# Optimization experiments

Hardware: AMD Instinct MI355X
Metric: run time of the kernel (lower is better)

Reference implementation:

```python
import jax, jax.numpy as jnp
import numpy as np


def setup_inputs() -> dict:
    key = jax.random.key(0)
    B, H, S, D = 4, 16, 2048, 128  # batch, kv heads, seq_len, head_dim
    kv_cache = jax.random.normal(key, (B, H, S, D), dtype=jnp.float32)
    return {"kv_cache": kv_cache, "rank": 64}


def reference(kv_cache, rank):
    # compress(): batched reduced SVD, truncate to `rank` components.
    orig_shape = kv_cache.shape
    S_len, D = orig_shape[-2], orig_shape[-1]
    x = kv_cache.reshape(-1, S_len, D)                 # [N, S, D]
    U, s, Vh = jnp.linalg.svd(x, full_matrices=False)  # U:[N,S,D], s:[N,D], Vh:[N,D,D]
    U_t = U[:, :, :rank]                               # [N, S, r]
    s_t = s[:, :rank]                                  # [N, r]
    Vh_t = Vh[:, :rank, :]                             # [N, r, D]
    left = U_t * s_t[:, None, :]                       # [N, S, r]  (= U * diag(s))
    # decompress(): left @ right^T, right = V[:, :, :rank] so right^T = Vh_t
    reconstructed = jnp.matmul(left, Vh_t)             # [N, S, D]
    return reconstructed.reshape(orig_shape)
```

## Files before the change

kernel.cpp:

```cpp
#include <hip/hip_runtime.h>


#define NM 64
#define SEQ 2048
#define DD 128
#define RR 64
#define NSWEEP 7
#define NROUND (NSWEEP * 64)

#define OFF_VFULL (4194304ULL)
#define OFF_NORM  (8388608ULL)
#define OFF_VT    (33554432ULL)

__device__ __forceinline__ float dot4(float4 a, float4 b) {
  return a.x * b.x + a.y * b.y + a.z * b.z + a.w * b.w;
}

template <int CTRL>
__device__ __forceinline__ float dpp_add(float x) {
  int y = __builtin_amdgcn_update_dpp(0, __float_as_int(x), CTRL, 0xf, 0xf, true);
  return x + __int_as_float(y);
}
__device__ __forceinline__ float red8(float x) {
  x = dpp_add<0xB1>(x);
  x = dpp_add<0x4E>(x);
  x = dpp_add<0x141>(x);
  return x;
}

__device__ __forceinline__ void jrot(float app, float apq, float aqq,
                                     float& c, float& s) {
  c = 1.f;
  s = 0.f;
  if (apq * apq > 1e-9f * app * aqq) {
    float tau = (aqq - app) / (2.f * apq);
    float tv = 1.f / (fabsf(tau) + sqrtf(1.f + tau * tau));
    tv = tau < 0.f ? -tv : tv;
    c = 1.f / sqrtf(1.f + tv * tv);
    s = tv * c;
  }
}

__device__ __forceinline__ void rot4(float c, float s, float4 p, float4 q,
                                     float4& np, float4& nq) {
  np.x = c * p.x - s * q.x;  nq.x = s * p.x + c * q.x;
  np.y = c * p.y - s * q.y;  nq.y = s * p.y + c * q.y;
  np.z = c * p.z - s * q.z;  nq.z = s * p.z + c * q.z;
  np.w = c * p.w - s * q.w;  nq.w = s * p.w + c * q.w;
}

__global__ __launch_bounds__(256) void gram_k(const float* __restrict__ X,
                                              float* __restrict__ G) {
  const int m = blockIdx.y;
  const int r0 = blockIdx.x * 32;
  const int tid = threadIdx.x;
  __shared__ __align__(16) float Xs[64][128];
  const float* Xm = X + (size_t)m * SEQ * DD;
  const int ti = tid >> 5;
  const int tj = tid & 31;
  float acc[4][4];
#pragma unroll
  for (int a = 0; a < 4; ++a)
#pragma unroll
    for (int b = 0; b < 4; ++b) acc[a][b] = 0.f;

  for (int s0 = 0; s0 < SEQ; s0 += 64) {
    __syncthreads();
    for (int t = tid; t < 2048; t += 256) {
      int s = t >> 5, c4 = t & 31;
      *(float4*)&Xs[s][c4 * 4] =
          *(const float4*)&Xm[(size_t)(s0 + s) * DD + c4 * 4];
    }
    __syncthreads();
#pragma unroll 4
    for (int s = 0; s < 64; ++s) {
      float4 av = *(const float4*)&Xs[s][r0 + 4 * ti];
      float4 bv = *(const float4*)&Xs[s][4 * tj];
      acc[0][0] += av.x * bv.x; acc[0][1] += av.x * bv.y;
      acc[0][2] += av.x * bv.z; acc[0][3] += av.x * bv.w;
      acc[1][0] += av.y * bv.x; acc[1][1] += av.y * bv.y;
      acc[1][2] += av.y * bv.z; acc[1][3] += av.y * bv.w;
      acc[2][0] += av.z * bv.x; acc[2][1] += av.z * bv.y;
      acc[2][2] += av.z * bv.z; acc[2][3] += av.z * bv.w;
      acc[3][0] += av.w * bv.x; acc[3][1] += av.w * bv.y;
      acc[3][2] += av.w * bv.z; acc[3][3] += av.w * bv.w;
    }
  }
  float* Gm = G + (size_t)m * DD * DD;
#pragma unroll
  for (int a = 0; a < 4; ++a) {
    float4 v = make_float4(acc[a][0], acc[a][1], acc[a][2], acc[a][3]);
    *(float4*)&Gm[(size_t)(r0 + 4 * ti + a) * DD + 4 * tj] = v;
  }
}

__global__ __launch_bounds__(512) void jacobi_oe_k(const float* __restrict__ G,
                                                   float* __restrict__ Vfull,
                                                   float* __restrict__ normg) {
  const int m = blockIdx.x;
  const int tid = threadIdx.x;
  const int g = tid >> 3;
  const int l = tid & 7;
  __shared__ float4 xch[DD * 32];

  const float4* Gm4 = (const float4*)(G + (size_t)m * DD * DD);
  float4 ce[4], co[4];
#pragma unroll
  for (int j = 0; j < 4; ++j) {
    ce[j] = Gm4[(size_t)(2 * g) * 32 + l + 8 * j];
    co[j] = Gm4[(size_t)(2 * g + 1) * 32 + l + 8 * j];
  }
  const bool hasR = (g < 63);
  const bool hasL = (g > 0);
  float4* homeE = &xch[(2 * g) * 32];
  float4* homeR = &xch[(2 * g + 2) * 32];

  for (int round = 0; round < NROUND; ++round) {
    {
      float app = 0.f, apq = 0.f, aqq = 0.f;
#pragma unroll
      for (int j = 0; j < 4; ++j) {
        app += dot4(ce[j], ce[j]);
        apq += dot4(ce[j], co[j]);
        aqq += dot4(co[j], co[j]);
      }
      app = red8(app); apq = red8(apq); aqq = red8(aqq);
      float c, s;
      jrot(app, apq, aqq, c, s);
#pragma unroll
      for (int j = 0; j < 4; ++j) {
        float4 np, nq;
        rot4(c, s, ce[j], co[j], np, nq);
        ce[j] = nq;
        co[j] = np;
      }
    }
    if (hasL) {
#pragma unroll
      for (int j = 0; j < 4; ++j) homeE[l + 8 * j] = ce[j];
    }
    __syncthreads();
    if (hasR) {
      float4 r[4];
#pragma unroll
      for (int j = 0; j < 4; ++j) r[j] = homeR[l + 8 * j];
      float app = 0.f, apq = 0.f, aqq = 0.f;
#pragma unroll
      for (int j = 0; j < 4; ++j) {
        app += dot4(co[j], co[j]);
        apq += dot4(co[j], r[j]);
        aqq += dot4(r[j], r[j]);
      }
      app = red8(app); apq = red8(apq); aqq = red8(aqq);
      float c, s;
      jrot(app, apq, aqq, c, s);
#pragma unroll
      for (int j = 0; j < 4; ++j) {
        float4 np, nq;
        rot4(c, s, co[j], r[j], np, nq);
        homeR[l + 8 * j] = np;
        co[j] = nq;
      }
    }
    __syncthreads();
    if (hasL) {
#pragma unroll
      for (int j = 0; j < 4; ++j) ce[j] = homeE[l + 8 * j];
    }
  }

  float ne = 0.f, no = 0.f;
#pragma unroll
  for (int j = 0; j < 4; ++j) {
    ne += dot4(ce[j], ce[j]);
    no += dot4(co[j], co[j]);
  }
  ne = red8(ne);
  no = red8(no);
  float4* Ve = (float4*)(Vfull + ((size_t)m * DD + 2 * g) * DD);
  float4* Vo = (float4*)(Vfull + ((size_t)m * DD + 2 * g + 1) * DD);
#pragma unroll
  for (int j = 0; j < 4; ++j) {
    Ve[l + 8 * j] = ce[j];
    Vo[l + 8 * j] = co[j];
  }
  if (l == 0) {
    normg[m * DD + 2 * g] = ne;
    normg[m * DD + 2 * g + 1] = no;
  }
}

__global__ __launch_bounds__(128) void select_k(const float* __restrict__ Vfull,
                                                const float* __restrict__ normg,
                                                float* __restrict__ Vt) {
  const int m = blockIdx.x;
  const int t = threadIdx.x;
  __shared__ float n[DD];
  __shared__ int inv[RR];
  __shared__ float scl[RR];
  n[t] = normg[m * DD + t];
  __syncthreads();
  float nt = n[t];
  int rk = 0;
  for (int k = 0; k < DD; ++k) {
    float nk = n[k];
    rk += ((nk > nt) || (nk == nt && k < t)) ? 1 : 0;
  }
  if (rk < RR) { inv[rk] = t; scl[rk] = 1.f / sqrtf(nt); }
  __syncthreads();
  for (int r = 0; r < RR; ++r) {
    Vt[((size_t)m * RR + r) * DD + t] =
        Vfull[((size_t)m * DD + inv[r]) * DD + t] * scl[r];
  }
}

__global__ __launch_bounds__(256) void gemm1_k(const float* __restrict__ X,
                                               const float* __restrict__ Vt,
                                               float* __restrict__ W) {
  const int m = blockIdx.y;
  const int s0 = blockIdx.x * 32;
  const int tid = threadIdx.x;
  __shared__ __align__(16) float VtT[128 * 68];
  __shared__ __align__(16) float Xs[32 * 132];
  const float* Vm = Vt + (size_t)m * RR * DD;
  for (int t = tid; t < RR * DD; t += 256) {
    int r = t >> 7, c = t & 127;
    VtT[c * 68 + r] = Vm[t];
  }
  const float* Xm = X + ((size_t)m * SEQ + s0) * DD;
  for (int t = tid; t < 1024; t += 256) {
    int s = t >> 5, c4 = t & 31;
    *(float4*)&Xs[s * 132 + 4 * c4] = *(const float4*)&Xm[(size_t)s * DD + 4 * c4];
  }
  __syncthreads();
  const int ti = tid >> 4;
  const int tj = tid & 15;
  float acc[2][4] = {{0.f, 0.f, 0.f, 0.f}, {0.f, 0.f, 0.f, 0.f}};
#pragma unroll 4
  for (int k = 0; k < DD; ++k) {
    float a0 = Xs[(2 * ti) * 132 + k];
    float a1 = Xs[(2 * ti + 1) * 132 + k];
    float4 bv = *(float4*)&VtT[k * 68 + 4 * tj];
    acc[0][0] += a0 * bv.x; acc[0][1] += a0 * bv.y;
    acc[0][2] += a0 * bv.z; acc[0][3] += a0 * bv.w;
    acc[1][0] += a1 * bv.x; acc[1][1] += a1 * bv.y;
    acc[1][2] += a1 * bv.z; acc[1][3] += a1 * bv.w;
  }
  float* Wm = W + ((size_t)m * SEQ + s0) * RR;
#pragma unroll
  for (int d = 0; d < 2; ++d) {
    float4 v = make_float4(acc[d][0], acc[d][1], acc[d][2], acc[d][3]);
    *(float4*)&Wm[(size_t)(2 * ti + d) * RR + 4 * tj] = v;
  }
}

__global__ __launch_bounds__(256) void gemm2_k(const float* __restrict__ W,
                                               const float* __restrict__ Vt,
                                               float* __restrict__ out) {
  const int m = blockIdx.y;
  const int s0 = blockIdx.x * 32;
  const int tid = threadIdx.x;
  __shared__ __align__(16) float Vts[64 * 132];
  __shared__ __align__(16) float Ws[32 * 68];
  const float* Vm = Vt + (size_t)m * RR * DD;
  for (int t = tid; t < 2048; t += 256) {
    int r = t >> 5, c4 = t & 31;
    *(float4*)&Vts[r * 132 + 4 * c4] = *(const float4*)&Vm[(size_t)r * DD + 4 * c4];
  }
  const float* Wm = W + ((size_t)m * SEQ + s0) * RR;
  for (int t = tid; t < 512; t += 256) {
    int s = t >> 4, c4 = t & 15;
    *(float4*)&Ws[s * 68 + 4 * c4] = *(const float4*)&Wm[(size_t)s * RR + 4 * c4];
  }
  __syncthreads();
  const int ti = tid >> 5;
  const int tj = tid & 31;
  float acc[4][4] = {{0.f,0.f,0.f,0.f},{0.f,0.f,0.f,0.f},
                     {0.f,0.f,0.f,0.f},{0.f,0.f,0.f,0.f}};
#pragma unroll 4
  for (int k = 0; k < RR; ++k) {
    float4 bv = *(float4*)&Vts[k * 132 + 4 * tj];
    float a0 = Ws[(4 * ti + 0) * 68 + k];
    float a1 = Ws[(4 * ti + 1) * 68 + k];
    float a2 = Ws[(4 * ti + 2) * 68 + k];
    float a3 = Ws[(4 * ti + 3) * 68 + k];
    acc[0][0] += a0 * bv.x; acc[0][1] += a0 * bv.y;
    acc[0][2] += a0 * bv.z; acc[0][3] += a0 * bv.w;
    acc[1][0] += a1 * bv.x; acc[1][1] += a1 * bv.y;
    acc[1][2] += a1 * bv.z; acc[1][3] += a1 * bv.w;
    acc[2][0] += a2 * bv.x; acc[2][1] += a2 * bv.y;
    acc[2][2] += a2 * bv.z; acc[2][3] += a2 * bv.w;
    acc[3][0] += a3 * bv.x; acc[3][1] += a3 * bv.y;
    acc[3][2] += a3 * bv.z; acc[3][3] += a3 * bv.w;
  }
  float* Om = out + ((size_t)m * SEQ + s0) * DD;
#pragma unroll
  for (int d = 0; d < 4; ++d) {
    float4 v = make_float4(acc[d][0], acc[d][1], acc[d][2], acc[d][3]);
    *(float4*)&Om[(size_t)(4 * ti + d) * DD + 4 * tj] = v;
  }
}

extern "C" void kernel_launch(void* const* d_in, const int* in_sizes, int n_in,
                              void* d_out, int out_size, void* d_ws, size_t ws_size,
                              hipStream_t stream) {
  (void)in_sizes; (void)n_in; (void)out_size; (void)ws_size;
  const float* X = (const float*)d_in[0];
  float* out = (float*)d_out;
  char* ws = (char*)d_ws;
  float* G = (float*)ws;
  float* Vfull = (float*)(ws + OFF_VFULL);
  float* normg = (float*)(ws + OFF_NORM);
  float* Vt = (float*)(ws + OFF_VT);
  float* W = (float*)ws;

  gram_k<<<dim3(4, NM), 256, 0, stream>>>(X, G);
  jacobi_oe_k<<<NM, 512, 0, stream>>>(G, Vfull, normg);
  select_k<<<NM, 128, 0, stream>>>(Vfull, normg, Vt);
  gemm1_k<<<dim3(SEQ / 32, NM), 256, 0, stream>>>(X, Vt, W);
  gemm2_k<<<dim3(SEQ / 32, NM), 256, 0, stream>>>(W, Vt, out);
}
```

Baseline: 1.132 ms.

## Replace odd-even Jacobi with hierarchical block Jacobi using wave-local exchanges

Replaces the flat odd-even one-sided Jacobi (448 rounds, each with two block-wide barriers) with a hierarchical scheme. Each 64-thread wavefront runs intra-block odd-even and ring rotations among its 16 columns, synchronising through LDS with only an lgkmcnt wait and no block barrier. Block-wide __syncthreads is needed only when blocks are swapped between waves in a 16-block tournament. This cuts the barrier count sharply and skips rotation arithmetic when the off-diagonal term is negligible, at the cost of a different sweep ordering and possibly different convergence or accuracy with the same cycle count.

Result: slower. 1.212 ms (+7.1%).

```diff
diff --git a/kernel.cpp b/kernel.cpp
--- a/kernel.cpp
+++ b/kernel.cpp
@@ -5,8 +5,7 @@
 #define SEQ 2048
 #define DD 128
 #define RR 64
-#define NSWEEP 7
-#define NROUND (NSWEEP * 64)
+#define NCYC 7
 
 #define OFF_VFULL (4194304ULL)
 #define OFF_NORM  (8388608ULL)
@@ -28,17 +27,20 @@
   return x;
 }
 
-__device__ __forceinline__ void jrot(float app, float apq, float aqq,
+__device__ __forceinline__ void waitlds() {
+  asm volatile("s_waitcnt lgkmcnt(0)" ::: "memory");
+  __builtin_amdgcn_sched_barrier(0);
+}
+
+__device__ __forceinline__ bool jrot(float app, float apq, float aqq,
                                      float& c, float& s) {
-  c = 1.f;
-  s = 0.f;
-  if (apq * apq > 1e-9f * app * aqq) {
-    float tau = (aqq - app) / (2.f * apq);
-    float tv = 1.f / (fabsf(tau) + sqrtf(1.f + tau * tau));
-    tv = tau < 0.f ? -tv : tv;
-    c = 1.f / sqrtf(1.f + tv * tv);
-    s = tv * c;
-  }
+  if (apq * apq <= 1e-9f * app * aqq) return false;
+  float tau = (aqq - app) / (2.f * apq);
+  float tv = 1.f / (fabsf(tau) + sqrtf(1.f + tau * tau));
+  tv = tau < 0.f ? -tv : tv;
+  c = 1.f / sqrtf(1.f + tv * tv);
+  s = tv * c;
+  return true;
 }
 
 __device__ __forceinline__ void rot4(float c, float s, float4 p, float4 q,
@@ -94,99 +96,166 @@
   }
 }
 
-__global__ __launch_bounds__(512) void jacobi_oe_k(const float* __restrict__ G,
-                                                   float* __restrict__ Vfull,
-                                                   float* __restrict__ normg) {
+__global__ __launch_bounds__(512) void jacobi_hier_k(const float* __restrict__ G,
+                                                     float* __restrict__ Vfull,
+                                                     float* __restrict__ normg) {
   const int m = blockIdx.x;
   const int tid = threadIdx.x;
-  const int g = tid >> 3;
+  const int W = tid >> 6;
+  const int o = (tid >> 3) & 7;
   const int l = tid & 7;
-  __shared__ float4 xch[DD * 32];
+  __shared__ float4 buf[4096];
+  float4* M = &buf[W * 264];
 
   const float4* Gm4 = (const float4*)(G + (size_t)m * DD * DD);
   float4 ce[4], co[4];
 #pragma unroll
   for (int j = 0; j < 4; ++j) {
-    ce[j] = Gm4[(size_t)(2 * g) * 32 + l + 8 * j];
-    co[j] = Gm4[(size_t)(2 * g + 1) * 32 + l + 8 * j];
-  }
-  const bool hasR = (g < 63);
-  const bool hasL = (g > 0);
-  float4* homeE = &xch[(2 * g) * 32];
-  float4* homeR = &xch[(2 * g + 2) * 32];
-
-  for (int round = 0; round < NROUND; ++round) {
-    {
-      float app = 0.f, apq = 0.f, aqq = 0.f;
+    ce[j] = Gm4[(size_t)(8 * W + o) * 32 + l + 8 * j];
+    co[j] = Gm4[(size_t)(8 * (15 - W) + o) * 32 + l + 8 * j];
+  }
+  const int dst_ce = (W == 0) ? 0 : W + 1;
+  const int dst_co = (W == 0) ? 1 : 16 - W;
+
+#pragma unroll 1
+  for (int cyc = 0; cyc < NCYC; ++cyc) {
+#pragma unroll 1
+    for (int r = 0; r < 8; ++r) {
+      {
+        float app = 0.f, apq = 0.f, aqq = 0.f;
+#pragma unroll
+        for (int j = 0; j < 4; ++j) {
+          app += dot4(ce[j], ce[j]);
+          apq += dot4(ce[j], co[j]);
+          aqq += dot4(co[j], co[j]);
+        }
+        app = red8(app); apq = red8(apq); aqq = red8(aqq);
+        float c, s;
+        if (jrot(app, apq, aqq, c, s)) {
+#pragma unroll
+          for (int j = 0; j < 4; ++j) {
+            float4 np, nq;
+            rot4(c, s, ce[j], co[j], np, nq);
+            ce[j] = nq; co[j] = np;
+          }
+        } else {
+#pragma unroll
+          for (int j = 0; j < 4; ++j) { float4 t = ce[j]; ce[j] = co[j]; co[j] = t; }
+        }
+      }
+      if (o > 0) {
+#pragma unroll
+        for (int j = 0; j < 4; ++j) M[o * 33 + l + 8 * j] = ce[j];
+      }
+      waitlds();
+      if (o < 7) {
+        float4 r4[4];
+#pragma unroll
+        for (int j = 0; j < 4; ++j) r4[j] = M[(o + 1) * 33 + l + 8 * j];
+        float app = 0.f, apq = 0.f, aqq = 0.f;
+#pragma unroll
+        for (int j = 0; j < 4; ++j) {
+          app += dot4(co[j], co[j]);
+          apq += dot4(co[j], r4[j]);
+          aqq += dot4(r4[j], r4[j]);
+        }
+        app = red8(app); apq = red8(apq); aqq = red8(aqq);
+        float c, s;
+        if (jrot(app, apq, aqq, c, s)) {
+#pragma unroll
+          for (int j = 0; j < 4; ++j) {
+            float4 np, nq;
+            rot4(c, s, co[j], r4[j], np, nq);
+            M[(o + 1) * 33 + l + 8 * j] = np;
+            co[j] = nq;
+          }
+        } else {
+#pragma unroll
+          for (int j = 0; j < 4; ++j) {
+            M[(o + 1) * 33 + l + 8 * j] = co[j];
+            co[j] = r4[j];
+          }
+        }
+      }
+      waitlds();
+      if (o > 0) {
+#pragma unroll
+        for (int j = 0; j < 4; ++j) ce[j] = M[o * 33 + l + 8 * j];
+      }
+    }
+#pragma unroll
+    for (int j = 0; j < 4; ++j) { float4 t = ce[j]; ce[j] = co[j]; co[j] = t; }
+
+#pragma unroll 1
+    for (int st = 0; st < 15; ++st) {
+      float4 qv[4];
+#pragma unroll
+      for (int j = 0; j < 4; ++j) qv[j] = co[j];
+#pragma unroll 1
+      for (int k = 0; k < 8; ++k) {
+        float app = 0.f, apq = 0.f, aqq = 0.f;
+#pragma unroll
+        for (int j = 0; j < 4; ++j) {
+          app += dot4(ce[j], ce[j]);
+          apq += dot4(ce[j], qv[j]);
+          aqq += dot4(qv[j], qv[j]);
+        }
+        app = red8(app); apq = red8(apq); aqq = red8(aqq);
+        float c, s;
+        if (jrot(app, apq, aqq, c, s)) {
+#pragma unroll
+          for (int j = 0; j < 4; ++j) {
+            float4 np, nq;
+            rot4(c, s, ce[j], qv[j], np, nq);
+            ce[j] = np; qv[j] = nq;
+          }
+        }
+        if (k < 7) {
+#pragma unroll
+          for (int j = 0; j < 4; ++j) M[o * 33 + l + 8 * j] = qv[j];
+          waitlds();
+#pragma unroll
+          for (int j = 0; j < 4; ++j) qv[j] = M[((o + 1) & 7) * 33 + l + 8 * j];
+        }
+      }
+#pragma unroll
+      for (int j = 0; j < 4; ++j) co[j] = qv[j];
+
+      __syncthreads();
 #pragma unroll
       for (int j = 0; j < 4; ++j) {
-        app += dot4(ce[j], ce[j]);
-        apq += dot4(ce[j], co[j]);
-        aqq += dot4(co[j], co[j]);
-      }
-      app = red8(app); apq = red8(apq); aqq = red8(aqq);
-      float c, s;
-      jrot(app, apq, aqq, c, s);
+        buf[dst_ce * 256 + o * 32 + l + 8 * j] = ce[j];
+        buf[dst_co * 256 + o * 32 + l + 8 * j] = co[j];
+      }
+      __syncthreads();
 #pragma unroll
       for (int j = 0; j < 4; ++j) {
-        float4 np, nq;
-        rot4(c, s, ce[j], co[j], np, nq);
-        ce[j] = nq;
-        co[j] = np;
-      }
+        ce[j] = buf[W * 256 + o * 32 + l + 8 * j];
+        co[j] = buf[(15 - W) * 256 + o * 32 + l + 8 * j];
+      }
+      __syncthreads();
     }
-    if (hasL) {
-#pragma unroll
-      for (int j = 0; j < 4; ++j) homeE[l + 8 * j] = ce[j];
-    }
-    __syncthreads();
-    if (hasR) {
-      float4 r[4];
-#pragma unroll
-      for (int j = 0; j < 4; ++j) r[j] = homeR[l + 8 * j];
-      float app = 0.f, apq = 0.f, aqq = 0.f;
-#pragma unroll
-      for (int j = 0; j < 4; ++j) {
-        app += dot4(co[j], co[j]);
-        apq += dot4(co[j], r[j]);
-        aqq += dot4(r[j], r[j]);
-      }
-      app = red8(app); apq = red8(apq); aqq = red8(aqq);
-      float c, s;
-      jrot(app, apq, aqq, c, s);
-#pragma unroll
-      for (int j = 0; j < 4; ++j) {
-        float4 np, nq;
-        rot4(c, s, co[j], r[j], np, nq);
-        homeR[l + 8 * j] = np;
-        co[j] = nq;
-      }
-    }
-    __syncthreads();
-    if (hasL) {
-#pragma unroll
-      for (int j = 0; j < 4; ++j) ce[j] = homeE[l + 8 * j];
-    }
-  }
-
-  float ne = 0.f, no = 0.f;
+  }
+
+  float ne = 0.f, no_ = 0.f;
 #pragma unroll
   for (int j = 0; j < 4; ++j) {
     ne += dot4(ce[j], ce[j]);
-    no += dot4(co[j], co[j]);
+    no_ += dot4(co[j], co[j]);
   }
   ne = red8(ne);
-  no = red8(no);
-  float4* Ve = (float4*)(Vfull + ((size_t)m * DD + 2 * g) * DD);
-  float4* Vo = (float4*)(Vfull + ((size_t)m * DD + 2 * g + 1) * DD);
+  no_ = red8(no_);
+  const int ie = W * 16 + 2 * o;
+  float4* Ve = (float4*)(Vfull + ((size_t)m * DD + ie) * DD);
+  float4* Vo = (float4*)(Vfull + ((size_t)m * DD + ie + 1) * DD);
 #pragma unroll
   for (int j = 0; j < 4; ++j) {
     Ve[l + 8 * j] = ce[j];
     Vo[l + 8 * j] = co[j];
   }
   if (l == 0) {
-    normg[m * DD + 2 * g] = ne;
-    normg[m * DD + 2 * g + 1] = no;
+    normg[m * DD + ie] = ne;
+    normg[m * DD + ie + 1] = no_;
   }
 }
 
@@ -315,7 +384,7 @@
   float* W = (float*)ws;
 
   gram_k<<<dim3(4, NM), 256, 0, stream>>>(X, G);
-  jacobi_oe_k<<<NM, 512, 0, stream>>>(G, Vfull, normg);
+  jacobi_hier_k<<<NM, 512, 0, stream>>>(G, Vfull, normg);
   select_k<<<NM, 128, 0, stream>>>(Vfull, normg, Vt);
   gemm1_k<<<dim3(SEQ / 32, NM), 256, 0, stream>>>(X, Vt, W);
   gemm2_k<<<dim3(SEQ / 32, NM), 256, 0, stream>>>(W, Vt, out);
```

## Process two matrices per Jacobi block and make rotation computation branch-free

Applied to the files above, without the earlier changes.

The Jacobi eigen-solver kernel now handles two independent Gram matrices per 512-thread block, interleaving their dot products, reductions and rotations so each barrier and DPP-reduction latency is amortized over twice the independent work. The exchange buffer is also halved to hold only even columns per matrix. The rotation helper is rewritten with selects instead of a branch to avoid divergence. The cost is double register pressure per thread and only 32 blocks launched, which leaves many CUs idle on a 256-CU device.

After: 2.035 ms. +79.8%, slower.

```diff
diff --git a/kernel.cpp b/kernel.cpp
--- a/kernel.cpp
+++ b/kernel.cpp
@@ -30,15 +30,15 @@
 
 __device__ __forceinline__ void jrot(float app, float apq, float aqq,
                                      float& c, float& s) {
-  c = 1.f;
-  s = 0.f;
-  if (apq * apq > 1e-9f * app * aqq) {
-    float tau = (aqq - app) / (2.f * apq);
-    float tv = 1.f / (fabsf(tau) + sqrtf(1.f + tau * tau));
-    tv = tau < 0.f ? -tv : tv;
-    c = 1.f / sqrtf(1.f + tv * tv);
-    s = tv * c;
-  }
+  bool ok = apq * apq > 1e-9f * app * aqq;
+  float ap = ok ? apq : 1.f;
+  float tau = (aqq - app) / (2.f * ap);
+  float tv = 1.f / (fabsf(tau) + sqrtf(1.f + tau * tau));
+  tv = tau < 0.f ? -tv : tv;
+  float cc = 1.f / sqrtf(1.f + tv * tv);
+  float ss = tv * cc;
+  c = ok ? cc : 1.f;
+  s = ok ? ss : 0.f;
 }
 
 __device__ __forceinline__ void rot4(float c, float s, float4 p, float4 q,
@@ -94,99 +94,133 @@
   }
 }
 
-__global__ __launch_bounds__(512) void jacobi_oe_k(const float* __restrict__ G,
-                                                   float* __restrict__ Vfull,
-                                                   float* __restrict__ normg) {
-  const int m = blockIdx.x;
+__global__ __launch_bounds__(512) void jacobi2_k(const float* __restrict__ G,
+                                                 float* __restrict__ Vfull,
+                                                 float* __restrict__ normg) {
+  const int m0 = 2 * blockIdx.x;
+  const int m1 = 2 * blockIdx.x + 1;
   const int tid = threadIdx.x;
   const int g = tid >> 3;
   const int l = tid & 7;
-  __shared__ float4 xch[DD * 32];
-
-  const float4* Gm4 = (const float4*)(G + (size_t)m * DD * DD);
-  float4 ce[4], co[4];
+  __shared__ __align__(16) float4 xA[RR * 32];
+  __shared__ __align__(16) float4 xB[RR * 32];
+
+  const float4* GA = (const float4*)(G + (size_t)m0 * DD * DD);
+  const float4* GB = (const float4*)(G + (size_t)m1 * DD * DD);
+  float4 ceA[4], coA[4], ceB[4], coB[4];
 #pragma unroll
   for (int j = 0; j < 4; ++j) {
-    ce[j] = Gm4[(size_t)(2 * g) * 32 + l + 8 * j];
-    co[j] = Gm4[(size_t)(2 * g + 1) * 32 + l + 8 * j];
+    ceA[j] = GA[(size_t)(2 * g) * 32 + l + 8 * j];
+    coA[j] = GA[(size_t)(2 * g + 1) * 32 + l + 8 * j];
+    ceB[j] = GB[(size_t)(2 * g) * 32 + l + 8 * j];
+    coB[j] = GB[(size_t)(2 * g + 1) * 32 + l + 8 * j];
   }
   const bool hasR = (g < 63);
   const bool hasL = (g > 0);
-  float4* homeE = &xch[(2 * g) * 32];
-  float4* homeR = &xch[(2 * g + 2) * 32];
+  float4* hEA = &xA[g * 32];
+  float4* hRA = &xA[(g + 1) * 32];
+  float4* hEB = &xB[g * 32];
+  float4* hRB = &xB[(g + 1) * 32];
 
   for (int round = 0; round < NROUND; ++round) {
     {
-      float app = 0.f, apq = 0.f, aqq = 0.f;
-#pragma unroll
-      for (int j = 0; j < 4; ++j) {
-        app += dot4(ce[j], ce[j]);
-        apq += dot4(ce[j], co[j]);
-        aqq += dot4(co[j], co[j]);
-      }
-      app = red8(app); apq = red8(apq); aqq = red8(aqq);
-      float c, s;
-      jrot(app, apq, aqq, c, s);
+      float apA = 0.f, aqA = 0.f, axA = 0.f;
+      float apB = 0.f, aqB = 0.f, axB = 0.f;
+#pragma unroll
+      for (int j = 0; j < 4; ++j) {
+        apA += dot4(ceA[j], ceA[j]); axA += dot4(ceA[j], coA[j]);
+        aqA += dot4(coA[j], coA[j]);
+        apB += dot4(ceB[j], ceB[j]); axB += dot4(ceB[j], coB[j]);
+        aqB += dot4(coB[j], coB[j]);
+      }
+      apA = red8(apA); axA = red8(axA); aqA = red8(aqA);
+      apB = red8(apB); axB = red8(axB); aqB = red8(aqB);
+      float cA, sA, cB, sB;
+      jrot(apA, axA, aqA, cA, sA);
+      jrot(apB, axB, aqB, cB, sB);
 #pragma unroll
       for (int j = 0; j < 4; ++j) {
         float4 np, nq;
-        rot4(c, s, ce[j], co[j], np, nq);
-        ce[j] = nq;
-        co[j] = np;
+        rot4(cA, sA, ceA[j], coA[j], np, nq);
+        ceA[j] = nq; coA[j] = np;
+        rot4(cB, sB, ceB[j], coB[j], np, nq);
+        ceB[j] = nq; coB[j] = np;
       }
     }
     if (hasL) {
 #pragma unroll
-      for (int j = 0; j < 4; ++j) homeE[l + 8 * j] = ce[j];
+      for (int j = 0; j < 4; ++j) {
+        hEA[l + 8 * j] = ceA[j];
+        hEB[l + 8 * j] = ceB[j];
+      }
     }
     __syncthreads();
     if (hasR) {
-      float4 r[4];
-#pragma unroll
-      for (int j = 0; j < 4; ++j) r[j] = homeR[l + 8 * j];
-      float app = 0.f, apq = 0.f, aqq = 0.f;
-#pragma unroll
-      for (int j = 0; j < 4; ++j) {
-        app += dot4(co[j], co[j]);
-        apq += dot4(co[j], r[j]);
-        aqq += dot4(r[j], r[j]);
-      }
-      app = red8(app); apq = red8(apq); aqq = red8(aqq);
-      float c, s;
-      jrot(app, apq, aqq, c, s);
+      float4 rA[4], rB[4];
+#pragma unroll
+      for (int j = 0; j < 4; ++j) {
+        rA[j] = hRA[l + 8 * j];
+        rB[j] = hRB[l + 8 * j];
+      }
+      float apA = 0.f, aqA = 0.f, axA = 0.f;
+      float apB = 0.f, aqB = 0.f, axB = 0.f;
+#pragma unroll
+      for (int j = 0; j < 4; ++j) {
+        apA += dot4(coA[j], coA[j]); axA += dot4(coA[j], rA[j]);
+        aqA += dot4(rA[j], rA[j]);
+        apB += dot4(coB[j], coB[j]); axB += dot4(coB[j], rB[j]);
+        aqB += dot4(rB[j], rB[j]);
+      }
+      apA = red8(apA); axA = red8(axA); aqA = red8(aqA);
+      apB = red8(apB); axB = red8(axB); aqB = red8(aqB);
+      float cA, sA, cB, sB;
+      jrot(apA, axA, aqA, cA, sA);
+      jrot(apB, axB, aqB, cB, sB);
 #pragma unroll
       for (int j = 0; j < 4; ++j) {
         float4 np, nq;
-        rot4(c, s, co[j], r[j], np, nq);
-        homeR[l + 8 * j] = np;
-        co[j] = nq;
+        rot4(cA, sA, coA[j], rA[j], np, nq);
+        hRA[l + 8 * j] = np;
+        coA[j] = nq;
+        rot4(cB, sB, coB[j], rB[j], np, nq);
+        hRB[l + 8 * j] = np;
+        coB[j] = nq;
       }
     }
     __syncthreads();
     if (hasL) {
 #pragma unroll
-      for (int j = 0; j < 4; ++j) ce[j] = homeE[l + 8 * j];
-    }
-  }
-
-  float ne = 0.f, no = 0.f;
+      for (int j = 0; j < 4; ++j) {
+        ceA[j] = hEA[l + 8 * j];
+        ceB[j] = hEB[l + 8 * j];
+      }
+    }
+  }
+
+  float nA0 = 0.f, nA1 = 0.f, nB0 = 0.f, nB1 = 0.f;
 #pragma unroll
   for (int j = 0; j < 4; ++j) {
-    ne += dot4(ce[j], ce[j]);
-    no += dot4(co[j], co[j]);
-  }
-  ne = red8(ne);
-  no = red8(no);
-  float4* Ve = (float4*)(Vfull + ((size_t)m * DD + 2 * g) * DD);
-  float4* Vo = (float4*)(Vfull + ((size_t)m * DD + 2 * g + 1) * DD);
+    nA0 += dot4(ceA[j], ceA[j]); nA1 += dot4(coA[j], coA[j]);
+    nB0 += dot4(ceB[j], ceB[j]); nB1 += dot4(coB[j], coB[j]);
+  }
+  nA0 = red8(nA0); nA1 = red8(nA1);
+  nB0 = red8(nB0); nB1 = red8(nB1);
+  float4* VeA = (float4*)(Vfull + ((size_t)m0 * DD + 2 * g) * DD);
+  float4* VoA = (float4*)(Vfull + ((size_t)m0 * DD + 2 * g + 1) * DD);
+  float4* VeB = (float4*)(Vfull + ((size_t)m1 * DD + 2 * g) * DD);
+  float4* VoB = (float4*)(Vfull + ((size_t)m1 * DD + 2 * g + 1) * DD);
 #pragma unroll
   for (int j = 0; j < 4; ++j) {
-    Ve[l + 8 * j] = ce[j];
-    Vo[l + 8 * j] = co[j];
+    VeA[l + 8 * j] = ceA[j];
+    VoA[l + 8 * j] = coA[j];
+    VeB[l + 8 * j] = ceB[j];
+    VoB[l + 8 * j] = coB[j];
   }
   if (l == 0) {
-    normg[m * DD + 2 * g] = ne;
-    normg[m * DD + 2 * g + 1] = no;
+    normg[m0 * DD + 2 * g] = nA0;
+    normg[m0 * DD + 2 * g + 1] = nA1;
+    normg[m1 * DD + 2 * g] = nB0;
+    normg[m1 * DD + 2 * g + 1] = nB1;
   }
 }
 
@@ -315,7 +349,7 @@
   float* W = (float*)ws;
 
   gram_k<<<dim3(4, NM), 256, 0, stream>>>(X, G);
-  jacobi_oe_k<<<NM, 512, 0, stream>>>(G, Vfull, normg);
+  jacobi2_k<<<NM / 2, 512, 0, stream>>>(G, Vfull, normg);
   select_k<<<NM, 128, 0, stream>>>(Vfull, normg, Vt);
   gemm1_k<<<dim3(SEQ / 32, NM), 256, 0, stream>>>(X, Vt, W);
   gemm2_k<<<dim3(SEQ / 32, NM), 256, 0, stream>>>(W, Vt, out);
```

## Track Jacobi column norms incrementally and cut sweep count in eigensolver

Applied to the files above, without the earlier changes.

The one-sided Jacobi kernel stops recomputing both column norms with dot products and reductions at every rotation. It updates them analytically from the rotation tangent and passes the neighbour's norm through a small shared array, so each pair needs only one dot product and one reduction. The sweep count also drops from 7 to 6, and jrot becomes branch-free using selects. The cost is norm drift in fp32 over many rotations and possibly less converged eigenvectors from fewer sweeps, which could hurt accuracy of the truncated reconstruction.

Measured after the change: 909.5 us. 19.7% less time.

```diff
diff --git a/kernel.cpp b/kernel.cpp
--- a/kernel.cpp
+++ b/kernel.cpp
@@ -5,7 +5,7 @@
 #define SEQ 2048
 #define DD 128
 #define RR 64
-#define NSWEEP 7
+#define NSWEEP 6
 #define NROUND (NSWEEP * 64)
 
 #define OFF_VFULL (4194304ULL)
@@ -29,16 +29,17 @@
 }
 
 __device__ __forceinline__ void jrot(float app, float apq, float aqq,
-                                     float& c, float& s) {
-  c = 1.f;
-  s = 0.f;
-  if (apq * apq > 1e-9f * app * aqq) {
-    float tau = (aqq - app) / (2.f * apq);
-    float tv = 1.f / (fabsf(tau) + sqrtf(1.f + tau * tau));
-    tv = tau < 0.f ? -tv : tv;
-    c = 1.f / sqrtf(1.f + tv * tv);
-    s = tv * c;
-  }
+                                     float& c, float& s, float& tv) {
+  bool ok = apq * apq > 1e-9f * app * aqq;
+  float ap = ok ? apq : 1.f;
+  float tau = (aqq - app) / (2.f * ap);
+  float t = 1.f / (fabsf(tau) + sqrtf(1.f + tau * tau));
+  t = tau < 0.f ? -t : t;
+  float cc = 1.f / sqrtf(1.f + t * t);
+  float ss = t * cc;
+  c = ok ? cc : 1.f;
+  s = ok ? ss : 0.f;
+  tv = ok ? t : 0.f;
 }
 
 __device__ __forceinline__ void rot4(float c, float s, float4 p, float4 q,
@@ -94,14 +95,15 @@
   }
 }
 
-__global__ __launch_bounds__(512) void jacobi_oe_k(const float* __restrict__ G,
+__global__ __launch_bounds__(512) void jacobi_nc_k(const float* __restrict__ G,
                                                    float* __restrict__ Vfull,
                                                    float* __restrict__ normg) {
   const int m = blockIdx.x;
   const int tid = threadIdx.x;
   const int g = tid >> 3;
   const int l = tid & 7;
-  __shared__ float4 xch[DD * 32];
+  __shared__ __align__(16) float4 xch[RR * 32];
+  __shared__ float nrm[RR];
 
   const float4* Gm4 = (const float4*)(G + (size_t)m * DD * DD);
   float4 ce[4], co[4];
@@ -110,73 +112,81 @@
     ce[j] = Gm4[(size_t)(2 * g) * 32 + l + 8 * j];
     co[j] = Gm4[(size_t)(2 * g + 1) * 32 + l + 8 * j];
   }
+  float nce = 0.f, nco = 0.f;
+#pragma unroll
+  for (int j = 0; j < 4; ++j) {
+    nce += dot4(ce[j], ce[j]);
+    nco += dot4(co[j], co[j]);
+  }
+  nce = red8(nce);
+  nco = red8(nco);
+
   const bool hasR = (g < 63);
   const bool hasL = (g > 0);
-  float4* homeE = &xch[(2 * g) * 32];
-  float4* homeR = &xch[(2 * g + 2) * 32];
+  float4* hE = &xch[g * 32];
+  float4* hR = &xch[(g + 1) * 32];
 
   for (int round = 0; round < NROUND; ++round) {
     {
-      float app = 0.f, apq = 0.f, aqq = 0.f;
-#pragma unroll
-      for (int j = 0; j < 4; ++j) {
-        app += dot4(ce[j], ce[j]);
-        apq += dot4(ce[j], co[j]);
-        aqq += dot4(co[j], co[j]);
-      }
-      app = red8(app); apq = red8(apq); aqq = red8(aqq);
-      float c, s;
-      jrot(app, apq, aqq, c, s);
+      float apq = 0.f;
+#pragma unroll
+      for (int j = 0; j < 4; ++j) apq += dot4(ce[j], co[j]);
+      apq = red8(apq);
+      float c, s, tv;
+      jrot(nce, apq, nco, c, s, tv);
 #pragma unroll
       for (int j = 0; j < 4; ++j) {
         float4 np, nq;
         rot4(c, s, ce[j], co[j], np, nq);
-        ce[j] = nq;
-        co[j] = np;
+        ce[j] = nq; co[j] = np;
       }
+      float t = nce;
+      nce = nco + tv * apq;
+      nco = t - tv * apq;
     }
     if (hasL) {
 #pragma unroll
-      for (int j = 0; j < 4; ++j) homeE[l + 8 * j] = ce[j];
+      for (int j = 0; j < 4; ++j) hE[l + 8 * j] = ce[j];
+      if (l == 0) nrm[g] = nce;
     }
     __syncthreads();
     if (hasR) {
-      float4 r[4];
-#pragma unroll
-      for (int j = 0; j < 4; ++j) r[j] = homeR[l + 8 * j];
-      float app = 0.f, apq = 0.f, aqq = 0.f;
-#pragma unroll
-      for (int j = 0; j < 4; ++j) {
-        app += dot4(co[j], co[j]);
-        apq += dot4(co[j], r[j]);
-        aqq += dot4(r[j], r[j]);
-      }
-      app = red8(app); apq = red8(apq); aqq = red8(aqq);
-      float c, s;
-      jrot(app, apq, aqq, c, s);
+      float4 r4[4];
+#pragma unroll
+      for (int j = 0; j < 4; ++j) r4[j] = hR[l + 8 * j];
+      float nr = nrm[g + 1];
+      float apq = 0.f;
+#pragma unroll
+      for (int j = 0; j < 4; ++j) apq += dot4(co[j], r4[j]);
+      apq = red8(apq);
+      float c, s, tv;
+      jrot(nco, apq, nr, c, s, tv);
 #pragma unroll
       for (int j = 0; j < 4; ++j) {
         float4 np, nq;
-        rot4(c, s, co[j], r[j], np, nq);
-        homeR[l + 8 * j] = np;
+        rot4(c, s, co[j], r4[j], np, nq);
+        hR[l + 8 * j] = np;
         co[j] = nq;
       }
+      if (l == 0) nrm[g + 1] = nco - tv * apq;
+      nco = nr + tv * apq;
     }
     __syncthreads();
     if (hasL) {
 #pragma unroll
-      for (int j = 0; j < 4; ++j) ce[j] = homeE[l + 8 * j];
-    }
-  }
-
-  float ne = 0.f, no = 0.f;
+      for (int j = 0; j < 4; ++j) ce[j] = hE[l + 8 * j];
+      nce = nrm[g];
+    }
+  }
+
+  float ne = 0.f, no_ = 0.f;
 #pragma unroll
   for (int j = 0; j < 4; ++j) {
     ne += dot4(ce[j], ce[j]);
-    no += dot4(co[j], co[j]);
+    no_ += dot4(co[j], co[j]);
   }
   ne = red8(ne);
-  no = red8(no);
+  no_ = red8(no_);
   float4* Ve = (float4*)(Vfull + ((size_t)m * DD + 2 * g) * DD);
   float4* Vo = (float4*)(Vfull + ((size_t)m * DD + 2 * g + 1) * DD);
 #pragma unroll
@@ -186,7 +196,7 @@
   }
   if (l == 0) {
     normg[m * DD + 2 * g] = ne;
-    normg[m * DD + 2 * g + 1] = no;
+    normg[m * DD + 2 * g + 1] = no_;
   }
 }
 
@@ -315,7 +325,7 @@
   float* W = (float*)ws;
 
   gram_k<<<dim3(4, NM), 256, 0, stream>>>(X, G);
-  jacobi_oe_k<<<NM, 512, 0, stream>>>(G, Vfull, normg);
+  jacobi_nc_k<<<NM, 512, 0, stream>>>(G, Vfull, normg);
   select_k<<<NM, 128, 0, stream>>>(Vfull, normg, Vt);
   gemm1_k<<<dim3(SEQ / 32, NM), 256, 0, stream>>>(X, Vt, W);
   gemm2_k<<<dim3(SEQ / 32, NM), 256, 0, stream>>>(W, Vt, out);
```
